# Optimization experiments

Measured on AMD Instinct MI355X. Metric: run time of the kernel, lower is better.

## Reference

```python
import jax, jax.numpy as jnp
import numpy as np

NEG = jnp.float32(-1e30)  # finite stand-in for -inf in masked max
SLOPE = 0.01              # F.leaky_relu default negative slope


def _lrelu(v):
    return jnp.where(v >= 0, v, SLOPE * v)


def _mlp(pts, w1, b1, w2, b2, w3, b3):
    # pts: [2, N] -> [64, N]; 1x1 Conv1d == pointwise linear over channel dim
    z = _lrelu(w1 @ pts + b1[:, None])
    z = _lrelu(w2 @ z + b2[:, None])
    z = _lrelu(w3 @ z + b3[:, None])
    return z


def setup_inputs() -> dict:
    key = jax.random.key(0)
    ks = jax.random.split(key, 10)
    B, C, H, W = 4, 19, 256, 256
    x = jax.random.randint(ks[0], (B, C, H, W), 0, 2, dtype=jnp.int32)
    # grid exactly as in the torch module: meshgrid of two linspaces, flattened
    g = np.array(np.meshgrid(np.linspace(-1, 1, 256), np.linspace(-1, 1, 256),
                             sparse=False)).astype(np.float32)  # [2,256,256]
    grid = jnp.asarray(g.reshape(2, -1))  # [2, 65536]
    w1 = jax.random.normal(ks[1], (64, 2), jnp.float32) * 0.5
    b1 = jax.random.normal(ks[2], (64,), jnp.float32) * 0.1
    w2 = jax.random.normal(ks[3], (64, 64), jnp.float32) * 0.125
    b2 = jax.random.normal(ks[4], (64,), jnp.float32) * 0.1
    w3 = jax.random.normal(ks[5], (64, 64), jnp.float32) * 0.125
    b3 = jax.random.normal(ks[6], (64,), jnp.float32) * 0.1
    fcw = jax.random.normal(ks[7], (512, 64 * C), jnp.float32)
    fcb = jax.random.normal(ks[8], (512,), jnp.float32) * 0.1
    return {"x": x, "grid": grid, "w1": w1, "b1": b1, "w2": w2, "b2": b2,
            "w3": w3, "b3": b3, "fcw": fcw, "fcb": fcb}


def reference(x, grid, w1, b1, w2, b2, w3, b3, fcw, fcb):
    B, C = x.shape[0], x.shape[1]
    # Pointwise MLP on the shared grid once (grid identical for all b,c)
    feats = _mlp(grid, w1, b1, w2, b2, w3, b3)                 # [64, N]
    # Fallback feature for empty masks: MLP on a single zero point
    zero_feat = _mlp(jnp.zeros((2, 1), feats.dtype),
                     w1, b1, w2, b2, w3, b3)[:, 0]             # [64]
    mask = (x.reshape(B, C, -1) == 1)                          # [B, C, N]
    # Masked max over the ragged point sets, fully vectorized
    masked = jnp.where(mask[:, :, None, :], feats[None, None], NEG)
    z = jnp.max(masked, axis=-1)                               # [B, C, 64]
    empty = ~jnp.any(mask, axis=-1)                            # [B, C]
    z = jnp.where(empty[..., None], zero_feat, z)
    flat = z.reshape(B, C * 64)                                # channel-major cat
    # EqualLinear: weight scaled by 1/sqrt(in_dim) (lr_mul=1)
    scale = jnp.float32(1.0 / np.sqrt(C * 64))
    out = flat @ (fcw * scale).T + fcb                         # [B, 512]
    return jnp.repeat(out[:, None, :], 18, axis=1)             # [B, 18, 512]
```

## Files before the change

kernel.cpp:

```cpp
#include <hip/hip_runtime.h>

#define NPTS  65536
#define NBC   76
#define NREP  8
#define KEYN  4864

typedef _Float16 f16;
typedef __fp16   h16x2 __attribute__((ext_vector_type(2)));
typedef _Float16 f16x8 __attribute__((ext_vector_type(8)));
typedef float    f32x4 __attribute__((ext_vector_type(4)));

__device__ __forceinline__ float lrelu(float v) { return fmaxf(v, 0.01f * v); }

__device__ __forceinline__ unsigned pkrtz(float lo, float hi) {
  h16x2 p = __builtin_amdgcn_cvt_pkrtz(lo, hi);
  return __builtin_bit_cast(unsigned, p);
}
__device__ __forceinline__ unsigned pkey(unsigned u) {
  unsigned t = (u >> 15) & 0x00010001u;
  return u ^ (0x80008000u | (t * 0x7FFFu));
}
__device__ __forceinline__ unsigned pkmax(unsigned a, unsigned b) {
  unsigned d;
  asm("v_pk_max_u16 %0, %1, %2" : "=v"(d) : "v"(a), "v"(b));
  return d;
}
__device__ __forceinline__ unsigned sext1(unsigned x, int b) {
  return (unsigned)(((int)(x << (31 - b))) >> 31);
}
__device__ __forceinline__ f16x8 ldcvt8(const float* p) {
  float4 a = *(const float4*)p, b = *(const float4*)(p + 4);
  uint4 u = make_uint4(pkrtz(a.x, a.y), pkrtz(a.z, a.w),
                       pkrtz(b.x, b.y), pkrtz(b.z, b.w));
  return __builtin_bit_cast(f16x8, u);
}

__device__ __forceinline__ void mfma_layer_r(
    const f16x8* wr, const f16* __restrict__ B, const float* __restrict__ bias,
    int chq, int q, int pt0, int pt1, f32x4& acc0, f32x4& acc1)
{
  float4 bv = *(const float4*)(bias + chq);
  acc0 = (f32x4){bv.x, bv.y, bv.z, bv.w};
  acc1 = acc0;
  #pragma unroll
  for (int s = 0; s < 2; ++s) {
    int k0 = s * 32;
    f16x8 b0 = *(const f16x8*)&B[pt0 * 72 + k0 + q * 8];
    f16x8 b1 = *(const f16x8*)&B[pt1 * 72 + k0 + q * 8];
    acc0 = __builtin_amdgcn_mfma_f32_16x16x32_f16(wr[s], b0, acc0, 0, 0, 0);
    acc1 = __builtin_amdgcn_mfma_f32_16x16x32_f16(wr[s], b1, acc1, 0, 0, 0);
  }
}

__device__ __forceinline__ void layer1(
    f16* __restrict__ zA, const float* __restrict__ w1,
    const float* __restrict__ b1, int wv, int lane, float g0, float g1)
{
  unsigned uo[4];
  #pragma unroll
  for (int p = 0; p < 4; ++p) {
    int j = wv * 8 + p * 2;
    float z0 = lrelu(w1[2 * j] * g0 + w1[2 * j + 1] * g1 + b1[j]);
    float z1 = lrelu(w1[2 * j + 2] * g0 + w1[2 * j + 3] * g1 + b1[j + 1]);
    uo[p] = pkrtz(z0, z1);
  }
  *(uint4*)&zA[lane * 72 + wv * 8] = make_uint4(uo[0], uo[1], uo[2], uo[3]);
}

__device__ __forceinline__ void phaseB(
    const unsigned* __restrict__ zk, const unsigned* mlo, const unsigned* mhi,
    unsigned* uacc, int rw)
{
  #pragma unroll
  for (int np = 0; np < 16; ++np) {
    uint4 z4 = *(const uint4*)&zk[rw * 68 + np * 4];
    const int p = np * 4, pb = p & 31;
    #pragma unroll
    for (int ii = 0; ii < 5; ++ii) {
      unsigned m = (p < 32) ? mlo[ii] : mhi[ii];
      unsigned s0 = sext1(m, pb),     s1 = sext1(m, pb + 1);
      unsigned s2 = sext1(m, pb + 2), s3 = sext1(m, pb + 3);
      unsigned a = uacc[ii];
      a = pkmax(a, z4.x & s0); a = pkmax(a, z4.y & s1);
      a = pkmax(a, z4.z & s2); a = pkmax(a, z4.w & s3);
      uacc[ii] = a;
    }
  }
}

__global__ __launch_bounds__(512, 8) void kAB(
    const int* __restrict__ x, const float* __restrict__ grid,
    const float* __restrict__ w1, const float* __restrict__ b1,
    const float* __restrict__ w2, const float* __restrict__ b2,
    const float* __restrict__ w3, const float* __restrict__ b3,
    int* __restrict__ keys)
{
  __shared__ __align__(16) unsigned char smem[36864];
  __shared__ unsigned long long mb0[NBC], mb1[NBC];
  f16* zA0 = (f16*)(smem);
  f16* zA1 = (f16*)(smem + 9216);
  f16* zB0 = (f16*)(smem + 18432);
  f16* zB1 = (f16*)(smem + 27648);
  unsigned* zk0 = (unsigned*)(smem);
  unsigned* zk1 = (unsigned*)(smem + 9216);

  const int t = threadIdx.x, lane = t & 63, wv = t >> 6;
  const int n0 = blockIdx.x * 128;

  int xa[10];
  #pragma unroll
  for (int i = 0; i < 10; ++i) {
    int bc = wv + 8 * i;
    if (bc < NBC) xa[i] = x[(bc << 16) + n0 + lane];
  }

  float g0a = grid[n0 + lane],      g1a = grid[NPTS + n0 + lane];
  float g0b = grid[n0 + 64 + lane], g1b = grid[NPTS + n0 + 64 + lane];

  const int chb = (wv & 3) * 16, pth = (wv >> 2) * 32;
  const int c15 = lane & 15, q = lane >> 4;
  const int chq = chb + q * 4;
  const int pt0 = pth + c15, pt1 = pth + 16 + c15;
  const int r0 = chq >> 1;

  f16x8 wr2[2], wr3[2];
  {
    const int row = (chb + c15) * 64 + q * 8;
    wr2[0] = ldcvt8(w2 + row);  wr2[1] = ldcvt8(w2 + row + 32);
    wr3[0] = ldcvt8(w3 + row);  wr3[1] = ldcvt8(w3 + row + 32);
  }

  layer1(zA0, w1, b1, wv, lane, g0a, g1a);
  layer1(zA1, w1, b1, wv, lane, g0b, g1b);

  #pragma unroll
  for (int i = 0; i < 10; ++i) {
    int bc = wv + 8 * i;
    if (bc < NBC) {
      unsigned long long m = __ballot(xa[i] == 1);
      if (lane == 0) mb0[bc] = m;
    }
  }
  #pragma unroll
  for (int i = 0; i < 10; ++i) {
    int bc = wv + 8 * i;
    if (bc < NBC) xa[i] = x[(bc << 16) + n0 + 64 + lane];
  }
  __syncthreads();

  f32x4 a0, a1;
  mfma_layer_r(wr2, zA0, b2, chq, q, pt0, pt1, a0, a1);
  *(uint2*)&zB0[pt0 * 72 + chq] =
      make_uint2(pkrtz(lrelu(a0[0]), lrelu(a0[1])), pkrtz(lrelu(a0[2]), lrelu(a0[3])));
  *(uint2*)&zB0[pt1 * 72 + chq] =
      make_uint2(pkrtz(lrelu(a1[0]), lrelu(a1[1])), pkrtz(lrelu(a1[2]), lrelu(a1[3])));
  mfma_layer_r(wr2, zA1, b2, chq, q, pt0, pt1, a0, a1);
  *(uint2*)&zB1[pt0 * 72 + chq] =
      make_uint2(pkrtz(lrelu(a0[0]), lrelu(a0[1])), pkrtz(lrelu(a0[2]), lrelu(a0[3])));
  *(uint2*)&zB1[pt1 * 72 + chq] =
      make_uint2(pkrtz(lrelu(a1[0]), lrelu(a1[1])), pkrtz(lrelu(a1[2]), lrelu(a1[3])));
  __syncthreads();

  mfma_layer_r(wr3, zB0, b3, chq, q, pt0, pt1, a0, a1);
  zk0[r0 * 68 + pt0]       = pkey(pkrtz(lrelu(a0[0]), lrelu(a0[1])));
  zk0[(r0 + 1) * 68 + pt0] = pkey(pkrtz(lrelu(a0[2]), lrelu(a0[3])));
  zk0[r0 * 68 + pt1]       = pkey(pkrtz(lrelu(a1[0]), lrelu(a1[1])));
  zk0[(r0 + 1) * 68 + pt1] = pkey(pkrtz(lrelu(a1[2]), lrelu(a1[3])));
  mfma_layer_r(wr3, zB1, b3, chq, q, pt0, pt1, a0, a1);
  zk1[r0 * 68 + pt0]       = pkey(pkrtz(lrelu(a0[0]), lrelu(a0[1])));
  zk1[(r0 + 1) * 68 + pt0] = pkey(pkrtz(lrelu(a0[2]), lrelu(a0[3])));
  zk1[r0 * 68 + pt1]       = pkey(pkrtz(lrelu(a1[0]), lrelu(a1[1])));
  zk1[(r0 + 1) * 68 + pt1] = pkey(pkrtz(lrelu(a1[2]), lrelu(a1[3])));

  #pragma unroll
  for (int i = 0; i < 10; ++i) {
    int bc = wv + 8 * i;
    if (bc < NBC) {
      unsigned long long m = __ballot(xa[i] == 1);
      if (lane == 0) mb1[bc] = m;
    }
  }
  __syncthreads();

  const int rw = t & 31, bg = t >> 5;
  const int bc0 = bg * 5;

  unsigned uacc[5] = {0u, 0u, 0u, 0u, 0u};
  unsigned mlo[5], mhi[5];
  #pragma unroll
  for (int ii = 0; ii < 5; ++ii) {
    int bc = bc0 + ii;
    unsigned long long m = (bc < NBC) ? mb0[bc] : 0ull;
    mlo[ii] = (unsigned)m; mhi[ii] = (unsigned)(m >> 32);
  }
  phaseB(zk0, mlo, mhi, uacc, rw);
  #pragma unroll
  for (int ii = 0; ii < 5; ++ii) {
    int bc = bc0 + ii;
    unsigned long long m = (bc < NBC) ? mb1[bc] : 0ull;
    mlo[ii] = (unsigned)m; mhi[ii] = (unsigned)(m >> 32);
  }
  phaseB(zk1, mlo, mhi, uacc, rw);

  int* krep = keys + (blockIdx.x & (NREP - 1)) * KEYN;
  #pragma unroll
  for (int ii = 0; ii < 5; ++ii) {
    int bc = bc0 + ii;
    if (bc < NBC) {
      int lo = (int)(uacc[ii] & 0xFFFFu), hi = (int)(uacc[ii] >> 16);
      if (lo) atomicMax(&krep[bc * 64 + 2 * rw], lo);
      if (hi) atomicMax(&krep[bc * 64 + 2 * rw + 1], hi);
    }
  }
}

__global__ __launch_bounds__(256) void k2_fc(
    const int* __restrict__ keys,
    const float* __restrict__ b1, const float* __restrict__ w2,
    const float* __restrict__ b2, const float* __restrict__ w3,
    const float* __restrict__ b3,
    const float* __restrict__ fcw, const float* __restrict__ fcb,
    float* __restrict__ out)
{
  __shared__ float flat[4864];
  __shared__ float za[64], zb[64], zf[64];
  const int t = threadIdx.x;

  if (t < 64) za[t] = lrelu(b1[t]);
  __syncthreads();
  if (t < 64) {
    float s = b2[t];
    #pragma unroll 8
    for (int k = 0; k < 64; ++k) s += w2[t * 64 + k] * za[k];
    zb[t] = lrelu(s);
  }
  __syncthreads();
  if (t < 64) {
    float s = b3[t];
    #pragma unroll 8
    for (int k = 0; k < 64; ++k) s += w3[t * 64 + k] * zb[k];
    zf[t] = lrelu(s);
  }
  __syncthreads();

  for (int idx = t; idx < 4864; idx += 256) {
    int m = keys[idx];
    #pragma unroll
    for (int r = 1; r < NREP; ++r) m = max(m, keys[r * KEYN + idx]);
    unsigned um = (unsigned)m;
    float v;
    if (um - 1u < 0xFFFFu) {
      unsigned u = (um & 0x8000u) ? (um ^ 0x8000u) : (~um & 0xFFFFu);
      unsigned short us = (unsigned short)u;
      v = (float)__builtin_bit_cast(f16, us);
    } else {
      v = zf[idx & 63];
    }
    flat[idx] = v;
  }
  __syncthreads();

  const int wv = t >> 6, lane = t & 63;
  const int o = blockIdx.x * 4 + wv;
  const float* wrow = fcw + o * 1216;
  float fa0 = 0.f, fa1 = 0.f, fa2 = 0.f, fa3 = 0.f;
  #pragma unroll
  for (int i = 0; i < 19; ++i) {
    int jj = i * 64 + lane;
    float wvv = wrow[jj];
    fa0 += wvv * flat[jj];
    fa1 += wvv * flat[1216 + jj];
    fa2 += wvv * flat[2432 + jj];
    fa3 += wvv * flat[3648 + jj];
  }
  #pragma unroll
  for (int off = 32; off > 0; off >>= 1) {
    fa0 += __shfl_xor(fa0, off);
    fa1 += __shfl_xor(fa1, off);
    fa2 += __shfl_xor(fa2, off);
    fa3 += __shfl_xor(fa3, off);
  }
  const float scale = 0.028676966733820225f;
  float cb = fcb[o];
  if (lane < 18) {
    out[(0 * 18 + lane) * 512 + o] = fa0 * scale + cb;
    out[(1 * 18 + lane) * 512 + o] = fa1 * scale + cb;
    out[(2 * 18 + lane) * 512 + o] = fa2 * scale + cb;
    out[(3 * 18 + lane) * 512 + o] = fa3 * scale + cb;
  }
}

extern "C" void kernel_launch(void* const* d_in, const int* in_sizes, int n_in,
                              void* d_out, int out_size, void* d_ws, size_t ws_size,
                              hipStream_t stream)
{
  const int*   x    = (const int*)d_in[0];
  const float* grid = (const float*)d_in[1];
  const float* w1   = (const float*)d_in[2];
  const float* b1   = (const float*)d_in[3];
  const float* w2   = (const float*)d_in[4];
  const float* b2   = (const float*)d_in[5];
  const float* w3   = (const float*)d_in[6];
  const float* b3   = (const float*)d_in[7];
  const float* fcw  = (const float*)d_in[8];
  const float* fcb  = (const float*)d_in[9];
  float* out = (float*)d_out;

  int* keys = (int*)d_ws;

  hipLaunchKernelGGL(kAB, dim3(512), dim3(512), 0, stream,
                     x, grid, w1, b1, w2, b2, w3, b3, keys);
  hipLaunchKernelGGL(k2_fc, dim3(128), dim3(256), 0, stream,
                     keys, b1, w2, b2, w3, b3, fcw, fcb, out);
}
```

Baseline: 128.3 us.

## Process 64 points per block with 1024 blocks and pre-check atomic max targets

Each block now handles 64 points instead of 128, so the grid doubles to 1024 blocks and shared memory per block halves. Layer and masked-max phases run once per block rather than twice. Before issuing atomicMax, each thread reads the current key values and only issues the atomic when its value is larger, aiming to cut atomic traffic. The cost is twice as many blocks, each issuing its own atomics and a prior global read, plus more redundant weight loads per point.

Result: slower. 164.6 us (+28.3%).

```diff
diff --git a/kernel.cpp b/kernel.cpp
--- a/kernel.cpp
+++ b/kernel.cpp
@@ -52,25 +52,92 @@
   }
 }
 
-__device__ __forceinline__ void layer1(
-    f16* __restrict__ zA, const float* __restrict__ w1,
-    const float* __restrict__ b1, int wv, int lane, float g0, float g1)
-{
-  unsigned uo[4];
-  #pragma unroll
-  for (int p = 0; p < 4; ++p) {
-    int j = wv * 8 + p * 2;
-    float z0 = lrelu(w1[2 * j] * g0 + w1[2 * j + 1] * g1 + b1[j]);
-    float z1 = lrelu(w1[2 * j + 2] * g0 + w1[2 * j + 3] * g1 + b1[j + 1]);
-    uo[p] = pkrtz(z0, z1);
-  }
-  *(uint4*)&zA[lane * 72 + wv * 8] = make_uint4(uo[0], uo[1], uo[2], uo[3]);
-}
-
-__device__ __forceinline__ void phaseB(
-    const unsigned* __restrict__ zk, const unsigned* mlo, const unsigned* mhi,
-    unsigned* uacc, int rw)
-{
+__global__ __launch_bounds__(512, 8) void kAB(
+    const int* __restrict__ x, const float* __restrict__ grid,
+    const float* __restrict__ w1, const float* __restrict__ b1,
+    const float* __restrict__ w2, const float* __restrict__ b2,
+    const float* __restrict__ w3, const float* __restrict__ b3,
+    int* __restrict__ keys)
+{
+  __shared__ __align__(16) unsigned char smem[18432];
+  __shared__ unsigned long long mbits[NBC];
+  f16* zA = (f16*)(smem);
+  f16* zB = (f16*)(smem + 9216);
+  unsigned* zk = (unsigned*)(smem);
+
+  const int t = threadIdx.x, lane = t & 63, wv = t >> 6;
+  const int n0 = blockIdx.x * 64;
+
+  int xa[10];
+  #pragma unroll
+  for (int i = 0; i < 10; ++i) {
+    int bc = wv + 8 * i;
+    if (bc < NBC) xa[i] = x[(bc << 16) + n0 + lane];
+  }
+
+  float g0 = grid[n0 + lane], g1 = grid[NPTS + n0 + lane];
+
+  const int chb = (wv & 3) * 16, pth = (wv >> 2) * 32;
+  const int c15 = lane & 15, q = lane >> 4;
+  const int chq = chb + q * 4;
+  const int pt0 = pth + c15, pt1 = pth + 16 + c15;
+  const int r0 = chq >> 1;
+
+  f16x8 wr2[2], wr3[2];
+  {
+    const int row = (chb + c15) * 64 + q * 8;
+    wr2[0] = ldcvt8(w2 + row);  wr2[1] = ldcvt8(w2 + row + 32);
+    wr3[0] = ldcvt8(w3 + row);  wr3[1] = ldcvt8(w3 + row + 32);
+  }
+
+  {
+    unsigned uo[4];
+    #pragma unroll
+    for (int p = 0; p < 4; ++p) {
+      int j = wv * 8 + p * 2;
+      float z0 = lrelu(w1[2 * j] * g0 + w1[2 * j + 1] * g1 + b1[j]);
+      float z1 = lrelu(w1[2 * j + 2] * g0 + w1[2 * j + 3] * g1 + b1[j + 1]);
+      uo[p] = pkrtz(z0, z1);
+    }
+    *(uint4*)&zA[lane * 72 + wv * 8] = make_uint4(uo[0], uo[1], uo[2], uo[3]);
+  }
+
+  #pragma unroll
+  for (int i = 0; i < 10; ++i) {
+    int bc = wv + 8 * i;
+    if (bc < NBC) {
+      unsigned long long m = __ballot(xa[i] == 1);
+      if (lane == 0) mbits[bc] = m;
+    }
+  }
+  __syncthreads();
+
+  f32x4 a0, a1;
+  mfma_layer_r(wr2, zA, b2, chq, q, pt0, pt1, a0, a1);
+  *(uint2*)&zB[pt0 * 72 + chq] =
+      make_uint2(pkrtz(lrelu(a0[0]), lrelu(a0[1])), pkrtz(lrelu(a0[2]), lrelu(a0[3])));
+  *(uint2*)&zB[pt1 * 72 + chq] =
+      make_uint2(pkrtz(lrelu(a1[0]), lrelu(a1[1])), pkrtz(lrelu(a1[2]), lrelu(a1[3])));
+  __syncthreads();
+
+  mfma_layer_r(wr3, zB, b3, chq, q, pt0, pt1, a0, a1);
+  zk[r0 * 68 + pt0]       = pkey(pkrtz(lrelu(a0[0]), lrelu(a0[1])));
+  zk[(r0 + 1) * 68 + pt0] = pkey(pkrtz(lrelu(a0[2]), lrelu(a0[3])));
+  zk[r0 * 68 + pt1]       = pkey(pkrtz(lrelu(a1[0]), lrelu(a1[1])));
+  zk[(r0 + 1) * 68 + pt1] = pkey(pkrtz(lrelu(a1[2]), lrelu(a1[3])));
+  __syncthreads();
+
+  const int rw = t & 31, bg = t >> 5;
+  const int bc0 = bg * 5;
+
+  unsigned uacc[5] = {0u, 0u, 0u, 0u, 0u};
+  unsigned mlo[5], mhi[5];
+  #pragma unroll
+  for (int ii = 0; ii < 5; ++ii) {
+    int bc = bc0 + ii;
+    unsigned long long m = (bc < NBC) ? mbits[bc] : 0ull;
+    mlo[ii] = (unsigned)m; mhi[ii] = (unsigned)(m >> 32);
+  }
   #pragma unroll
   for (int np = 0; np < 16; ++np) {
     uint4 z4 = *(const uint4*)&zk[rw * 68 + np * 4];
@@ -86,130 +153,24 @@
       uacc[ii] = a;
     }
   }
-}
-
-__global__ __launch_bounds__(512, 8) void kAB(
-    const int* __restrict__ x, const float* __restrict__ grid,
-    const float* __restrict__ w1, const float* __restrict__ b1,
-    const float* __restrict__ w2, const float* __restrict__ b2,
-    const float* __restrict__ w3, const float* __restrict__ b3,
-    int* __restrict__ keys)
-{
-  __shared__ __align__(16) unsigned char smem[36864];
-  __shared__ unsigned long long mb0[NBC], mb1[NBC];
-  f16* zA0 = (f16*)(smem);
-  f16* zA1 = (f16*)(smem + 9216);
-  f16* zB0 = (f16*)(smem + 18432);
-  f16* zB1 = (f16*)(smem + 27648);
-  unsigned* zk0 = (unsigned*)(smem);
-  unsigned* zk1 = (unsigned*)(smem + 9216);
-
-  const int t = threadIdx.x, lane = t & 63, wv = t >> 6;
-  const int n0 = blockIdx.x * 128;
-
-  int xa[10];
-  #pragma unroll
-  for (int i = 0; i < 10; ++i) {
-    int bc = wv + 8 * i;
-    if (bc < NBC) xa[i] = x[(bc << 16) + n0 + lane];
-  }
-
-  float g0a = grid[n0 + lane],      g1a = grid[NPTS + n0 + lane];
-  float g0b = grid[n0 + 64 + lane], g1b = grid[NPTS + n0 + 64 + lane];
-
-  const int chb = (wv & 3) * 16, pth = (wv >> 2) * 32;
-  const int c15 = lane & 15, q = lane >> 4;
-  const int chq = chb + q * 4;
-  const int pt0 = pth + c15, pt1 = pth + 16 + c15;
-  const int r0 = chq >> 1;
-
-  f16x8 wr2[2], wr3[2];
-  {
-    const int row = (chb + c15) * 64 + q * 8;
-    wr2[0] = ldcvt8(w2 + row);  wr2[1] = ldcvt8(w2 + row + 32);
-    wr3[0] = ldcvt8(w3 + row);  wr3[1] = ldcvt8(w3 + row + 32);
-  }
-
-  layer1(zA0, w1, b1, wv, lane, g0a, g1a);
-  layer1(zA1, w1, b1, wv, lane, g0b, g1b);
-
-  #pragma unroll
-  for (int i = 0; i < 10; ++i) {
-    int bc = wv + 8 * i;
-    if (bc < NBC) {
-      unsigned long long m = __ballot(xa[i] == 1);
-      if (lane == 0) mb0[bc] = m;
-    }
-  }
-  #pragma unroll
-  for (int i = 0; i < 10; ++i) {
-    int bc = wv + 8 * i;
-    if (bc < NBC) xa[i] = x[(bc << 16) + n0 + 64 + lane];
-  }
-  __syncthreads();
-
-  f32x4 a0, a1;
-  mfma_layer_r(wr2, zA0, b2, chq, q, pt0, pt1, a0, a1);
-  *(uint2*)&zB0[pt0 * 72 + chq] =
-      make_uint2(pkrtz(lrelu(a0[0]), lrelu(a0[1])), pkrtz(lrelu(a0[2]), lrelu(a0[3])));
-  *(uint2*)&zB0[pt1 * 72 + chq] =
-      make_uint2(pkrtz(lrelu(a1[0]), lrelu(a1[1])), pkrtz(lrelu(a1[2]), lrelu(a1[3])));
-  mfma_layer_r(wr2, zA1, b2, chq, q, pt0, pt1, a0, a1);
-  *(uint2*)&zB1[pt0 * 72 + chq] =
-      make_uint2(pkrtz(lrelu(a0[0]), lrelu(a0[1])), pkrtz(lrelu(a0[2]), lrelu(a0[3])));
-  *(uint2*)&zB1[pt1 * 72 + chq] =
-      make_uint2(pkrtz(lrelu(a1[0]), lrelu(a1[1])), pkrtz(lrelu(a1[2]), lrelu(a1[3])));
-  __syncthreads();
-
-  mfma_layer_r(wr3, zB0, b3, chq, q, pt0, pt1, a0, a1);
-  zk0[r0 * 68 + pt0]       = pkey(pkrtz(lrelu(a0[0]), lrelu(a0[1])));
-  zk0[(r0 + 1) * 68 + pt0] = pkey(pkrtz(lrelu(a0[2]), lrelu(a0[3])));
-  zk0[r0 * 68 + pt1]       = pkey(pkrtz(lrelu(a1[0]), lrelu(a1[1])));
-  zk0[(r0 + 1) * 68 + pt1] = pkey(pkrtz(lrelu(a1[2]), lrelu(a1[3])));
-  mfma_layer_r(wr3, zB1, b3, chq, q, pt0, pt1, a0, a1);
-  zk1[r0 * 68 + pt0]       = pkey(pkrtz(lrelu(a0[0]), lrelu(a0[1])));
-  zk1[(r0 + 1) * 68 + pt0] = pkey(pkrtz(lrelu(a0[2]), lrelu(a0[3])));
-  zk1[r0 * 68 + pt1]       = pkey(pkrtz(lrelu(a1[0]), lrelu(a1[1])));
-  zk1[(r0 + 1) * 68 + pt1] = pkey(pkrtz(lrelu(a1[2]), lrelu(a1[3])));
-
-  #pragma unroll
-  for (int i = 0; i < 10; ++i) {
-    int bc = wv + 8 * i;
-    if (bc < NBC) {
-      unsigned long long m = __ballot(xa[i] == 1);
-      if (lane == 0) mb1[bc] = m;
-    }
-  }
-  __syncthreads();
-
-  const int rw = t & 31, bg = t >> 5;
-  const int bc0 = bg * 5;
-
-  unsigned uacc[5] = {0u, 0u, 0u, 0u, 0u};
-  unsigned mlo[5], mhi[5];
+
+  int* krep = keys + (blockIdx.x & (NREP - 1)) * KEYN;
+  int cur0[5], cur1[5];
   #pragma unroll
   for (int ii = 0; ii < 5; ++ii) {
     int bc = bc0 + ii;
-    unsigned long long m = (bc < NBC) ? mb0[bc] : 0ull;
-    mlo[ii] = (unsigned)m; mhi[ii] = (unsigned)(m >> 32);
-  }
-  phaseB(zk0, mlo, mhi, uacc, rw);
-  #pragma unroll
-  for (int ii = 0; ii < 5; ++ii) {
-    int bc = bc0 + ii;
-    unsigned long long m = (bc < NBC) ? mb1[bc] : 0ull;
-    mlo[ii] = (unsigned)m; mhi[ii] = (unsigned)(m >> 32);
-  }
-  phaseB(zk1, mlo, mhi, uacc, rw);
-
-  int* krep = keys + (blockIdx.x & (NREP - 1)) * KEYN;
+    if (bc < NBC) {
+      cur0[ii] = krep[bc * 64 + 2 * rw];
+      cur1[ii] = krep[bc * 64 + 2 * rw + 1];
+    }
+  }
   #pragma unroll
   for (int ii = 0; ii < 5; ++ii) {
     int bc = bc0 + ii;
     if (bc < NBC) {
       int lo = (int)(uacc[ii] & 0xFFFFu), hi = (int)(uacc[ii] >> 16);
-      if (lo) atomicMax(&krep[bc * 64 + 2 * rw], lo);
-      if (hi) atomicMax(&krep[bc * 64 + 2 * rw + 1], hi);
+      if (lo > cur0[ii]) atomicMax(&krep[bc * 64 + 2 * rw], lo);
+      if (hi > cur1[ii]) atomicMax(&krep[bc * 64 + 2 * rw + 1], hi);
     }
   }
 }
@@ -308,7 +269,7 @@
 
   int* keys = (int*)d_ws;
 
-  hipLaunchKernelGGL(kAB, dim3(512), dim3(512), 0, stream,
+  hipLaunchKernelGGL(kAB, dim3(1024), dim3(512), 0, stream,
                      x, grid, w1, b1, w2, b2, w3, b3, keys);
   hipLaunchKernelGGL(k2_fc, dim3(128), dim3(256), 0, stream,
                      keys, b1, w2, b2, w3, b3, fcw, fcb, out);
```
